# Performance work log

Measured on AMD Instinct MI355X. Metric: run time of the kernel, lower is better.

The kernel has to match this reference:

```python
import jax, jax.numpy as jnp
import numpy as np


def sparsemax(z):
    # z: [..., E] -> sparse probability simplex projection (Martins & Astudillo 2016).
    E = z.shape[-1]
    z_sorted = -jnp.sort(-z, axis=-1)                 # descending
    z_cum = jnp.cumsum(z_sorted, axis=-1)
    k = jnp.arange(1, E + 1, dtype=z.dtype)
    support = (1.0 + k * z_sorted) > z_cum            # [..., E] bool
    k_z = jnp.sum(support, axis=-1, keepdims=True)    # support size >= 1
    tau_sum = jnp.take_along_axis(z_cum, k_z.astype(jnp.int32) - 1, axis=-1)
    tau = (tau_sum - 1.0) / k_z.astype(z.dtype)
    return jnp.maximum(z - tau, 0.0)


def setup_inputs() -> dict:
    key = jax.random.key(0)
    ks = jax.random.split(key, 6)
    B, S, D_IN, D_OUT, E, R = 8, 2048, 4096, 4096, 8, 16
    x = jax.random.normal(ks[0], (B, S, D_IN), dtype=jnp.float32)
    W_base = jax.random.normal(ks[1], (D_OUT, D_IN), dtype=jnp.float32) * (D_IN ** -0.5)
    b_base = jax.random.normal(ks[2], (D_OUT,), dtype=jnp.float32) * 0.01
    W_router = jax.random.normal(ks[3], (E, D_IN), dtype=jnp.float32) * (D_IN ** -0.5)
    b_router = jnp.zeros((E,), dtype=jnp.float32)
    lora_A = jax.random.normal(ks[4], (E, D_IN, R), dtype=jnp.float32) * (D_IN ** -0.5)
    lora_B = jnp.zeros((E, R, D_OUT), dtype=jnp.float32)  # standard LoRA zero-init on B
    return {"x": x, "W_base": W_base, "b_base": b_base,
            "W_router": W_router, "b_router": b_router,
            "lora_A": lora_A, "lora_B": lora_B}


def reference(x, W_base, b_base, W_router, b_router, lora_A, lora_B):
    # Frozen base projection: [B,S,D_in] @ [D_in,D_out]
    base_out = jnp.einsum('bsd,od->bso', x, W_base) + b_base
    # Sparsegen (sparsemax) router over experts
    logits = jnp.einsum('bsd,ed->bse', x, W_router) + b_router
    weights = sparsemax(logits)                       # [B,S,E], mostly-sparse
    # LoRA experts: low-rank path per expert, summed with token-dependent weights
    h = jnp.einsum('bsd,edr->bser', x, lora_A)        # [B,S,E,R]
    expert_out = jnp.einsum('bser,bse,ero->bso', h, weights, lora_B)
    return base_out + expert_out
```

## Files before the change

kernel.cpp:

```cpp
#include <hip/hip_runtime.h>
#include <hip/hip_bf16.h>

#define M_TOK 16384
#define DK    4096
#define DN    4096
#define NE    8
#define NR    16
#define ERC   128
#define RAC   160
#define NT_MAIN 128
#define NT_ALL  132

typedef __attribute__((ext_vector_type(8))) short bfrag;
typedef __attribute__((ext_vector_type(4))) float f32x4;

__device__ __forceinline__ unsigned short f2bf(float f) {
  unsigned u = __builtin_bit_cast(unsigned, f);
  unsigned rounding = 0x7FFFu + ((u >> 16) & 1u);
  u += rounding;
  return (unsigned short)(u >> 16);
}

__device__ __forceinline__ void load_lds16(const void* g, void* l) {
  __builtin_amdgcn_global_load_lds(
      (__attribute__((address_space(1))) void*)(g),
      (__attribute__((address_space(3))) void*)(l), 16, 0, 0);
}

__global__ void k_cvt(const float* __restrict__ in, unsigned short* __restrict__ out, long n4) {
  long i = (long)blockIdx.x * blockDim.x + threadIdx.x;
  long stride = (long)gridDim.x * blockDim.x;
  for (; i < n4; i += stride) {
    float4 v = reinterpret_cast<const float4*>(in)[i];
    ushort4 o;
    o.x = f2bf(v.x); o.y = f2bf(v.y); o.z = f2bf(v.z); o.w = f2bf(v.w);
    reinterpret_cast<ushort4*>(out)[i] = o;
  }
}

__global__ void k_build_ra(const float* __restrict__ Wr, const float* __restrict__ lA,
                           unsigned short* __restrict__ RA) {
  int idx = blockIdx.x * 256 + threadIdx.x;
  if (idx >= RAC * DK) return;
  int c = idx >> 12;
  int k = idx & (DK - 1);
  float v = 0.f;
  if (c < NE) {
    v = Wr[c * DK + k];
  } else if (c < NE + ERC) {
    int er = c - NE;
    int e = er >> 4, r = er & 15;
    v = lA[((long)e * DK + k) * NR + r];
  }
  RA[idx] = f2bf(v);
}

__global__ void k_build_bt(const float* __restrict__ lB, unsigned short* __restrict__ BT) {
  int idx = blockIdx.x * 256 + threadIdx.x;
  if (idx >= DN * ERC) return;
  int n = idx >> 7;
  int kp = idx & 127;
  BT[idx] = f2bf(lB[(long)kp * DN + n]);
}

__global__ __launch_bounds__(256, 2)
void k_gemm_small(const unsigned short* __restrict__ X, const unsigned short* __restrict__ RA,
                  float* __restrict__ H) {
  __shared__ unsigned short At[64 * 64];
  __shared__ unsigned short Bt[RAC * 64];
  int m0 = blockIdx.x * 64;
  int tid = threadIdx.x;
  int lane = tid & 63, wid = tid >> 6;
  int wr = wid >> 1, wc = wid & 1;
  int l16 = lane & 15, lhi = lane >> 4;
  f32x4 acc[2][5] = {};
  int byteoff = tid * 16;
  for (int k0 = 0; k0 < DK; k0 += 64) {
#pragma unroll
    for (int r = 0; r < 2; r++) {
      int off = r * 4096 + byteoff;
      int row = off >> 7, colb = off & 127;
      load_lds16((const char*)X + ((long)(m0 + row) * DK + k0) * 2 + colb, (char*)At + off);
    }
#pragma unroll
    for (int r = 0; r < 5; r++) {
      int off = r * 4096 + byteoff;
      int row = off >> 7, colb = off & 127;
      load_lds16((const char*)RA + ((long)row * DK + k0) * 2 + colb, (char*)Bt + off);
    }
    __syncthreads();
#pragma unroll
    for (int kk = 0; kk < 2; kk++) {
      bfrag a[2], b[5];
#pragma unroll
      for (int m = 0; m < 2; m++)
        a[m] = *(const bfrag*)&At[(wr * 32 + m * 16 + l16) * 64 + kk * 32 + lhi * 8];
#pragma unroll
      for (int n = 0; n < 5; n++)
        b[n] = *(const bfrag*)&Bt[(wc * 80 + n * 16 + l16) * 64 + kk * 32 + lhi * 8];
#pragma unroll
      for (int m = 0; m < 2; m++)
#pragma unroll
        for (int n = 0; n < 5; n++)
          acc[m][n] = __builtin_amdgcn_mfma_f32_16x16x32_bf16(a[m], b[n], acc[m][n], 0, 0, 0);
    }
    __syncthreads();
  }
#pragma unroll
  for (int m = 0; m < 2; m++)
#pragma unroll
    for (int n = 0; n < 5; n++) {
      int col = wc * 80 + n * 16 + l16;
      int row = m0 + wr * 32 + m * 16 + lhi * 4;
#pragma unroll
      for (int j = 0; j < 4; j++)
        H[(long)(row + j) * RAC + col] = acc[m][n][j];
    }
}

__global__ void k_router(const float* __restrict__ H, const float* __restrict__ b_router,
                         unsigned short* __restrict__ G) {
  int t = blockIdx.x * blockDim.x + threadIdx.x;
  if (t >= M_TOK) return;
  const float* row = H + (long)t * RAC;
  float z[NE], zs[NE];
#pragma unroll
  for (int e = 0; e < NE; e++) { z[e] = row[e] + b_router[e]; zs[e] = z[e]; }
#pragma unroll
  for (int i = 1; i < NE; i++) {
    float key = zs[i];
    int j = i - 1;
    while (j >= 0 && zs[j] < key) { zs[j + 1] = zs[j]; j--; }
    zs[j + 1] = key;
  }
  float cums[NE];
  float cum = 0.f;
#pragma unroll
  for (int j = 0; j < NE; j++) { cum += zs[j]; cums[j] = cum; }
  int kz = 0;
#pragma unroll
  for (int j = 0; j < NE; j++)
    if (1.f + (float)(j + 1) * zs[j] > cums[j]) kz = j + 1;
  float tau = (cums[kz - 1] - 1.f) / (float)kz;
#pragma unroll
  for (int e = 0; e < NE; e++) {
    float we = fmaxf(z[e] - tau, 0.f);
#pragma unroll
    for (int r = 0; r < NR; r++)
      G[(long)t * ERC + e * NR + r] = f2bf(we * row[NE + e * NR + r]);
  }
}

struct KtArgs {
  const unsigned short *pXA0, *pXA1, *pWB0, *pWB1, *pGA0, *pGA1, *pTB0, *pTB1;
  int soffA0, soffA1, soffB0, soffB1;
  int wr, wc, l16, swslot;
};

template<bool STAGE, int VMB>
__device__ __forceinline__ void ktile_body(int t, unsigned short* lds, const KtArgs& A,
                                           f32x4 (&acc)[8][4]) {
  unsigned short* s = lds + (t & 3) * 16384;
  bfrag bfr[4], al[4], ah[4];
#pragma unroll
  for (int n = 0; n < 4; n++)
    bfr[n] = *(const bfrag*)&s[8192 + (A.wc * 64 + n * 16 + A.l16) * 32 + A.swslot];
#pragma unroll
  for (int m = 0; m < 4; m++)
    al[m] = *(const bfrag*)&s[(A.wr * 128 + m * 16 + A.l16) * 32 + A.swslot];
  if constexpr (STAGE) {
    int u = t + 3;
    unsigned short* d = lds + (u & 3) * 16384;
    if (u < NT_MAIN) {
      load_lds16(A.pXA0 + (long)u * 32, d + A.soffA0);
      load_lds16(A.pXA1 + (long)u * 32, d + A.soffA1);
    } else {
      long v = u - NT_MAIN;
      load_lds16(A.pGA0 + v * 32, d + A.soffA0);
      load_lds16(A.pGA1 + v * 32, d + A.soffA1);
    }
  }
  asm volatile("s_barrier\n\ts_waitcnt lgkmcnt(0)" ::: "memory");
  __builtin_amdgcn_sched_barrier(0);
  __builtin_amdgcn_s_setprio(1);
#pragma unroll
  for (int m = 0; m < 4; m++)
#pragma unroll
    for (int n = 0; n < 4; n++)
      acc[m][n] = __builtin_amdgcn_mfma_f32_16x16x32_bf16(al[m], bfr[n], acc[m][n], 0, 0, 0);
  __builtin_amdgcn_s_setprio(0);
#pragma unroll
  for (int m = 0; m < 4; m++)
    ah[m] = *(const bfrag*)&s[(A.wr * 128 + 64 + m * 16 + A.l16) * 32 + A.swslot];
  if constexpr (STAGE) {
    int u = t + 3;
    unsigned short* d = lds + (u & 3) * 16384;
    if (u < NT_MAIN) {
      load_lds16(A.pWB0 + (long)u * 32, d + A.soffB0);
      load_lds16(A.pWB1 + (long)u * 32, d + A.soffB1);
    } else {
      long v = u - NT_MAIN;
      load_lds16(A.pTB0 + v * 32, d + A.soffB0);
      load_lds16(A.pTB1 + v * 32, d + A.soffB1);
    }
  }
  asm volatile("s_barrier\n\ts_waitcnt lgkmcnt(0)" ::: "memory");
  __builtin_amdgcn_sched_barrier(0);
  __builtin_amdgcn_s_setprio(1);
#pragma unroll
  for (int m = 0; m < 4; m++)
#pragma unroll
    for (int n = 0; n < 4; n++)
      acc[4 + m][n] = __builtin_amdgcn_mfma_f32_16x16x32_bf16(ah[m], bfr[n], acc[4 + m][n], 0, 0, 0);
  __builtin_amdgcn_s_setprio(0);
  if constexpr (VMB == 8)      asm volatile("s_waitcnt vmcnt(8)\n\ts_barrier" ::: "memory");
  else if constexpr (VMB == 4) asm volatile("s_waitcnt vmcnt(4)\n\ts_barrier" ::: "memory");
  else if constexpr (VMB == 0) asm volatile("s_waitcnt vmcnt(0)\n\ts_barrier" ::: "memory");
}

__global__ __launch_bounds__(512, 2)
void k_gemm_main(const unsigned short* __restrict__ X, const unsigned short* __restrict__ W,
                 const unsigned short* __restrict__ G, const unsigned short* __restrict__ BT,
                 const float* __restrict__ bias, float* __restrict__ out) {
  __shared__ unsigned short lds[4 * 16384];
  int bid = blockIdx.x;
  int swz = (bid & 7) * 128 + (bid >> 3);
  int bm = swz >> 4, bn = swz & 15;
  int m0 = bm * 256, n0 = bn * 256;
  int tid = threadIdx.x;
  int lane = tid & 63, wid = tid >> 6;

  KtArgs A;
  A.wr = wid >> 2; A.wc = wid & 3;
  A.l16 = lane & 15;
  int lhi = lane >> 4;
  A.swslot = (lhi ^ ((A.l16 >> 1) & 3)) * 8;
  int r0 = tid >> 2;
  int c8 = (((tid & 3) ^ ((tid >> 3) & 3)) * 8);
  A.pXA0 = X + (long)(m0 + r0) * DK + c8;
  A.pXA1 = X + (long)(m0 + 128 + r0) * DK + c8;
  A.pWB0 = W + (long)(n0 + r0) * DK + c8;
  A.pWB1 = W + (long)(n0 + 128 + r0) * DK + c8;
  A.pGA0 = G + (long)(m0 + r0) * ERC + c8;
  A.pGA1 = G + (long)(m0 + 128 + r0) * ERC + c8;
  A.pTB0 = BT + (long)(n0 + r0) * ERC + c8;
  A.pTB1 = BT + (long)(n0 + 128 + r0) * ERC + c8;
  A.soffA0 = tid * 8;
  A.soffA1 = 4096 + tid * 8;
  A.soffB0 = 8192 + tid * 8;
  A.soffB1 = 12288 + tid * 8;

  f32x4 acc[8][4] = {};

#pragma unroll
  for (int u = 0; u < 3; u++) {
    unsigned short* d = lds + u * 16384;
    load_lds16(A.pXA0 + (long)u * 32, d + A.soffA0);
    load_lds16(A.pXA1 + (long)u * 32, d + A.soffA1);
    load_lds16(A.pWB0 + (long)u * 32, d + A.soffB0);
    load_lds16(A.pWB1 + (long)u * 32, d + A.soffB1);
  }
  asm volatile("s_waitcnt vmcnt(8)\n\ts_barrier" ::: "memory");

  for (int t = 0; t <= 128; t++)
    ktile_body<true, 8>(t, lds, A, acc);
  ktile_body<false, 4>(129, lds, A, acc);
  ktile_body<false, 0>(130, lds, A, acc);
  ktile_body<false, -1>(131, lds, A, acc);

#pragma unroll
  for (int n = 0; n < 4; n++) {
    int col = n0 + A.wc * 64 + n * 16 + A.l16;
    float bv = bias[col];
#pragma unroll
    for (int m = 0; m < 8; m++) {
      int row = m0 + A.wr * 128 + m * 16 + lhi * 4;
#pragma unroll
      for (int j = 0; j < 4; j++)
        out[(long)(row + j) * DN + col] = acc[m][n][j] + bv;
    }
  }
}

extern "C" void kernel_launch(void* const* d_in, const int* in_sizes, int n_in,
                              void* d_out, int out_size, void* d_ws, size_t ws_size,
                              hipStream_t stream) {
  const float* x        = (const float*)d_in[0];
  const float* W_base   = (const float*)d_in[1];
  const float* b_base   = (const float*)d_in[2];
  const float* W_router = (const float*)d_in[3];
  const float* b_router = (const float*)d_in[4];
  const float* lora_A   = (const float*)d_in[5];
  const float* lora_B   = (const float*)d_in[6];
  float* out = (float*)d_out;

  char* ws = (char*)d_ws;
  unsigned short* Xb = (unsigned short*)ws;
  unsigned short* Wb = (unsigned short*)(ws + 134217728L);
  unsigned short* RA = (unsigned short*)(ws + 167772160L);
  unsigned short* BT = (unsigned short*)(ws + 169082880L);
  float*          H  = (float*)(ws + 170131456L);
  unsigned short* G  = (unsigned short*)(ws + 180617216L);

  hipLaunchKernelGGL(k_cvt, dim3(2048), dim3(256), 0, stream, x, Xb, (long)M_TOK * DK / 4);
  hipLaunchKernelGGL(k_cvt, dim3(2048), dim3(256), 0, stream, W_base, Wb, (long)DN * DK / 4);
  hipLaunchKernelGGL(k_build_ra, dim3((RAC * DK + 255) / 256), dim3(256), 0, stream,
                     W_router, lora_A, RA);
  hipLaunchKernelGGL(k_build_bt, dim3((DN * ERC + 255) / 256), dim3(256), 0, stream, lora_B, BT);
  hipLaunchKernelGGL(k_gemm_small, dim3(M_TOK / 64), dim3(256), 0, stream, Xb, RA, H);
  hipLaunchKernelGGL(k_router, dim3(M_TOK / 256), dim3(256), 0, stream, H, b_router, G);
  hipLaunchKernelGGL(k_gemm_main, dim3((M_TOK / 256) * (DN / 256)), dim3(512), 0, stream,
                     Xb, Wb, G, BT, b_base, out);
}
```

Before: 709.5 us.

## Fuse x conversion, router GEMM and sparsemax into one small kernel

The small router/LoRA-A GEMM now reads fp32 x directly, converts it to bf16 in registers, writes the bf16 copy to global for the main GEMM and stages it in LDS. This removes the separate x conversion pass and its extra read of x. The sparsemax router and gating are also computed in-kernel from an LDS tile of H, so the H round-trip to global memory and the separate router launch go away. In exchange the kernel uses more LDS, which may lower occupancy, and x loading becomes a synchronous register path instead of async direct-to-LDS loads.

```diff
diff --git a/kernel.cpp b/kernel.cpp
--- a/kernel.cpp
+++ b/kernel.cpp
@@ -64,29 +64,46 @@
 }
 
 __global__ __launch_bounds__(256, 2)
-void k_gemm_small(const unsigned short* __restrict__ X, const unsigned short* __restrict__ RA,
-                  float* __restrict__ H) {
+void k_small_fused(const float* __restrict__ x, const unsigned short* __restrict__ RA,
+                   unsigned short* __restrict__ Xb, const float* __restrict__ b_router,
+                   unsigned short* __restrict__ Gout) {
   __shared__ unsigned short At[64 * 64];
   __shared__ unsigned short Bt[RAC * 64];
+  __shared__ float Hl[64][160];
+  __shared__ float Wl[64][NE];
   int m0 = blockIdx.x * 64;
   int tid = threadIdx.x;
   int lane = tid & 63, wid = tid >> 6;
   int wr = wid >> 1, wc = wid & 1;
   int l16 = lane & 15, lhi = lane >> 4;
   f32x4 acc[2][5] = {};
+  int row = tid >> 2, c16 = (tid & 3) * 16;
   int byteoff = tid * 16;
   for (int k0 = 0; k0 < DK; k0 += 64) {
-#pragma unroll
-    for (int r = 0; r < 2; r++) {
-      int off = r * 4096 + byteoff;
-      int row = off >> 7, colb = off & 127;
-      load_lds16((const char*)X + ((long)(m0 + row) * DK + k0) * 2 + colb, (char*)At + off);
-    }
+    const float* xs = x + (long)(m0 + row) * DK + k0 + c16;
+    float4 v0 = *(const float4*)(xs);
+    float4 v1 = *(const float4*)(xs + 4);
+    float4 v2 = *(const float4*)(xs + 8);
+    float4 v3 = *(const float4*)(xs + 12);
+    bfrag lo, hi;
+    lo[0] = (short)f2bf(v0.x); lo[1] = (short)f2bf(v0.y);
+    lo[2] = (short)f2bf(v0.z); lo[3] = (short)f2bf(v0.w);
+    lo[4] = (short)f2bf(v1.x); lo[5] = (short)f2bf(v1.y);
+    lo[6] = (short)f2bf(v1.z); lo[7] = (short)f2bf(v1.w);
+    hi[0] = (short)f2bf(v2.x); hi[1] = (short)f2bf(v2.y);
+    hi[2] = (short)f2bf(v2.z); hi[3] = (short)f2bf(v2.w);
+    hi[4] = (short)f2bf(v3.x); hi[5] = (short)f2bf(v3.y);
+    hi[6] = (short)f2bf(v3.z); hi[7] = (short)f2bf(v3.w);
+    unsigned short* xb = Xb + (long)(m0 + row) * DK + k0 + c16;
+    *(bfrag*)xb = lo;
+    *(bfrag*)(xb + 8) = hi;
+    *(bfrag*)&At[row * 64 + c16] = lo;
+    *(bfrag*)&At[row * 64 + c16 + 8] = hi;
 #pragma unroll
     for (int r = 0; r < 5; r++) {
       int off = r * 4096 + byteoff;
-      int row = off >> 7, colb = off & 127;
-      load_lds16((const char*)RA + ((long)row * DK + k0) * 2 + colb, (char*)Bt + off);
+      int rrow = off >> 7, colb = off & 127;
+      load_lds16((const char*)RA + ((long)rrow * DK + k0) * 2 + colb, (char*)Bt + off);
     }
     __syncthreads();
 #pragma unroll
@@ -111,43 +128,40 @@
 #pragma unroll
     for (int n = 0; n < 5; n++) {
       int col = wc * 80 + n * 16 + l16;
-      int row = m0 + wr * 32 + m * 16 + lhi * 4;
+      int trow = wr * 32 + m * 16 + lhi * 4;
 #pragma unroll
       for (int j = 0; j < 4; j++)
-        H[(long)(row + j) * RAC + col] = acc[m][n][j];
-    }
-}
-
-__global__ void k_router(const float* __restrict__ H, const float* __restrict__ b_router,
-                         unsigned short* __restrict__ G) {
-  int t = blockIdx.x * blockDim.x + threadIdx.x;
-  if (t >= M_TOK) return;
-  const float* row = H + (long)t * RAC;
-  float z[NE], zs[NE];
-#pragma unroll
-  for (int e = 0; e < NE; e++) { z[e] = row[e] + b_router[e]; zs[e] = z[e]; }
-#pragma unroll
-  for (int i = 1; i < NE; i++) {
-    float key = zs[i];
-    int j = i - 1;
-    while (j >= 0 && zs[j] < key) { zs[j + 1] = zs[j]; j--; }
-    zs[j + 1] = key;
-  }
-  float cums[NE];
-  float cum = 0.f;
-#pragma unroll
-  for (int j = 0; j < NE; j++) { cum += zs[j]; cums[j] = cum; }
-  int kz = 0;
-#pragma unroll
-  for (int j = 0; j < NE; j++)
-    if (1.f + (float)(j + 1) * zs[j] > cums[j]) kz = j + 1;
-  float tau = (cums[kz - 1] - 1.f) / (float)kz;
-#pragma unroll
-  for (int e = 0; e < NE; e++) {
-    float we = fmaxf(z[e] - tau, 0.f);
-#pragma unroll
-    for (int r = 0; r < NR; r++)
-      G[(long)t * ERC + e * NR + r] = f2bf(we * row[NE + e * NR + r]);
+        Hl[trow + j][col] = acc[m][n][j];
+    }
+  __syncthreads();
+  if (tid < 64) {
+    float z[NE], zs[NE];
+#pragma unroll
+    for (int e = 0; e < NE; e++) { z[e] = Hl[tid][e] + b_router[e]; zs[e] = z[e]; }
+#pragma unroll
+    for (int i = 1; i < NE; i++) {
+      float key = zs[i];
+      int j = i - 1;
+      while (j >= 0 && zs[j] < key) { zs[j + 1] = zs[j]; j--; }
+      zs[j + 1] = key;
+    }
+    float cums[NE];
+    float cum = 0.f;
+#pragma unroll
+    for (int j = 0; j < NE; j++) { cum += zs[j]; cums[j] = cum; }
+    int kz = 0;
+#pragma unroll
+    for (int j = 0; j < NE; j++)
+      if (1.f + (float)(j + 1) * zs[j] > cums[j]) kz = j + 1;
+    float tau = (cums[kz - 1] - 1.f) / (float)kz;
+#pragma unroll
+    for (int e = 0; e < NE; e++)
+      Wl[tid][e] = fmaxf(z[e] - tau, 0.f);
+  }
+  __syncthreads();
+  for (int idx = tid; idx < 64 * ERC; idx += 256) {
+    int tk = idx >> 7, er = idx & 127;
+    Gout[(long)(m0 + tk) * ERC + er] = f2bf(Wl[tk][er >> 4] * Hl[tk][NE + er]);
   }
 }
 
@@ -299,16 +313,14 @@
   unsigned short* Wb = (unsigned short*)(ws + 134217728L);
   unsigned short* RA = (unsigned short*)(ws + 167772160L);
   unsigned short* BT = (unsigned short*)(ws + 169082880L);
-  float*          H  = (float*)(ws + 170131456L);
   unsigned short* G  = (unsigned short*)(ws + 180617216L);
 
-  hipLaunchKernelGGL(k_cvt, dim3(2048), dim3(256), 0, stream, x, Xb, (long)M_TOK * DK / 4);
   hipLaunchKernelGGL(k_cvt, dim3(2048), dim3(256), 0, stream, W_base, Wb, (long)DN * DK / 4);
   hipLaunchKernelGGL(k_build_ra, dim3((RAC * DK + 255) / 256), dim3(256), 0, stream,
                      W_router, lora_A, RA);
   hipLaunchKernelGGL(k_build_bt, dim3((DN * ERC + 255) / 256), dim3(256), 0, stream, lora_B, BT);
-  hipLaunchKernelGGL(k_gemm_small, dim3(M_TOK / 64), dim3(256), 0, stream, Xb, RA, H);
-  hipLaunchKernelGGL(k_router, dim3(M_TOK / 256), dim3(256), 0, stream, H, b_router, G);
+  hipLaunchKernelGGL(k_small_fused, dim3(M_TOK / 64), dim3(256), 0, stream,
+                     x, RA, Xb, b_router, G);
   hipLaunchKernelGGL(k_gemm_main, dim3((M_TOK / 256) * (DN / 256)), dim3(512), 0, stream,
                      Xb, Wb, G, BT, b_base, out);
 }
```

Result: faster. 674.0 us (-5.0%).
